# Kernel optimization log

Measured on AMD Instinct MI355X. Metric: run time of the kernel, lower is better.

## Reference

```python
import jax, jax.numpy as jnp
import numpy as np

LENGTH = 5
TOP_K = 5
POOL_SIZE = 60
EMBED_DIM = 768
MAP_SCALE = 0.1
MAX_NORM = 1.0 - 4e-3  # Poincare ball projection eps for float32 (geoopt convention)
EPS = 1e-12


def _l2_normalize(x):
    ss = jnp.sum(x * x, axis=-1, keepdims=True)
    return x * jax.lax.rsqrt(jnp.maximum(ss, EPS))


def _expmap0(u):
    # c = 1: expmap0(u) = tanh(||u||) * u / ||u||
    n = jnp.sqrt(jnp.maximum(jnp.sum(u * u, axis=-1, keepdims=True), 1e-15))
    return jnp.tanh(n) * u / n


def _proju0(x):
    # project onto the open unit ball
    n = jnp.sqrt(jnp.maximum(jnp.sum(x * x, axis=-1, keepdims=True), 1e-15))
    return jnp.where(n > MAX_NORM, x * (MAX_NORM / n), x)


def _map_to_ball(x):
    return _proju0(_expmap0(_l2_normalize(x) * MAP_SCALE))


def _mobius_add(x, y):
    # c = 1 Mobius addition, broadcasting over leading dims
    x2 = jnp.sum(x * x, axis=-1, keepdims=True)
    y2 = jnp.sum(y * y, axis=-1, keepdims=True)
    xy = jnp.sum(x * y, axis=-1, keepdims=True)
    num = (1.0 + 2.0 * xy + y2) * x + (1.0 - x2) * y
    den = 1.0 + 2.0 * xy + x2 * y2
    return num / jnp.maximum(den, 1e-15)


def _poincare_dist(x, y):
    # dist(x, y) = 2 * artanh(||(-x) mobius+ y||)  (c = 1)
    d = _mobius_add(-x, y)
    n = jnp.sqrt(jnp.maximum(jnp.sum(d * d, axis=-1), 1e-15))
    n = jnp.clip(n, 0.0, 1.0 - 1e-7)
    return 2.0 * jnp.arctanh(n)


def setup_inputs() -> dict:
    key = jax.random.key(0)
    k1, k2, k3 = jax.random.split(key, 3)
    x_embed = jax.random.normal(k1, (128, 512, EMBED_DIM), dtype=jnp.float32)
    prompt = jax.random.uniform(k2, (POOL_SIZE, LENGTH, EMBED_DIM), dtype=jnp.float32, minval=-1.0, maxval=1.0)
    prompt_key = jax.random.uniform(k3, (POOL_SIZE, EMBED_DIM), dtype=jnp.float32, minval=-1.0, maxval=1.0)
    return {"x_embed": x_embed, "prompt": prompt, "prompt_key": prompt_key}


def reference(x_embed, prompt, prompt_key):
    B = x_embed.shape[0]
    x_mean = jnp.mean(x_embed, axis=1)                      # [B, D]
    key_ball = _map_to_ball(prompt_key)                     # [P, D]
    q_ball = _map_to_ball(x_mean)                           # [B, D]
    dist = _poincare_dist(q_ball[:, None, :], key_ball[None, :, :])  # [B, P]
    similarity = -dist
    _, idx = jax.lax.top_k(similarity, TOP_K)               # [B, K]
    idx = jnp.sort(idx, axis=1)
    batched_prompt = prompt[idx].reshape(B, TOP_K * LENGTH, EMBED_DIM)
    selected_key = key_ball[idx]                            # [B, K, D]
    selected_dist = jnp.take_along_axis(dist, idx, axis=1)  # [B, K]
    reduce_sim = jnp.sum(selected_dist) / B
    prompted_embedding = jnp.concatenate([batched_prompt, x_embed], axis=1)
    return (prompted_embedding, reduce_sim, idx, similarity, selected_key)
```

## Files before the change

### kernel.cpp

```cpp
#include <hip/hip_runtime.h>

#define EMBED   768
#define EMBED4  192
#define POOL    60
#define BATCH   128
#define SEQ     512
#define TOPK    5
#define LEN     5
#define OUTROWS 537
#define NSLICE  16

#define SZ_PE   (128L*537L*768L)
#define OFF_RS  (SZ_PE)
#define OFF_IDX (OFF_RS + 1)
#define OFF_SIM (OFF_IDX + 640)
#define OFF_SK  (OFF_SIM + 7680)

#define WS_PARTIAL 0
#define WS_KEYBALL 1572864
#define WS_KEYY2   1618944

#define MAX_NORM_F 0.996f

__device__ __forceinline__ float block_reduce_256(float v, float* red) {
    int tid = threadIdx.x;
    #pragma unroll
    for (int m = 32; m >= 1; m >>= 1) v += __shfl_xor(v, m, 64);
    if ((tid & 63) == 0) red[tid >> 6] = v;
    __syncthreads();
    float total = red[0] + red[1] + red[2] + red[3];
    __syncthreads();
    return total;
}

__global__ __launch_bounds__(192) void mean_partial_copy(
        const float* __restrict__ x, float* __restrict__ out, float* __restrict__ partial) {
    const int slice = blockIdx.x, b = blockIdx.y, tid = threadIdx.x;
    const float4* __restrict__ x4 = (const float4*)x;
    float4* __restrict__ out4 = (float4*)out;
    float4* __restrict__ p4 = (float4*)partial;

    if (slice == 0 && b == 0 && tid == 0) out[OFF_RS] = 0.0f;

    float4 acc = make_float4(0.f, 0.f, 0.f, 0.f);
    const int rows = SEQ / NSLICE;
    const long ibase = ((long)b * SEQ + slice * rows) * EMBED4 + tid;
    const long obase = ((long)b * OUTROWS + 25 + slice * rows) * EMBED4 + tid;
    #pragma unroll 4
    for (int s = 0; s < rows; ++s) {
        float4 v = x4[ibase + (long)s * EMBED4];
        acc.x += v.x; acc.y += v.y; acc.z += v.z; acc.w += v.w;
        out4[obase + (long)s * EMBED4] = v;
    }
    p4[(long)(b * NSLICE + slice) * EMBED4 + tid] = acc;
}

__global__ __launch_bounds__(256) void keyball_kernel(
        const float* __restrict__ pkey, float* __restrict__ keyball, float* __restrict__ keyy2) {
    __shared__ float red[4];
    const int p = blockIdx.x, tid = threadIdx.x;
    float v[3];
    float ss = 0.f;
    #pragma unroll
    for (int j = 0; j < 3; ++j) { v[j] = pkey[p * EMBED + tid + 256 * j]; ss += v[j] * v[j]; }
    ss = block_reduce_256(ss, red);
    const float scale1 = rsqrtf(fmaxf(ss, 1e-12f)) * 0.1f;
    float su = 0.f;
    #pragma unroll
    for (int j = 0; j < 3; ++j) { v[j] *= scale1; su += v[j] * v[j]; }
    su = block_reduce_256(su, red);
    const float n = sqrtf(fmaxf(su, 1e-15f));
    const float f = tanhf(n) / n;
    float sb = 0.f;
    #pragma unroll
    for (int j = 0; j < 3; ++j) { v[j] *= f; sb += v[j] * v[j]; }
    sb = block_reduce_256(sb, red);
    const float n2 = sqrtf(fmaxf(sb, 1e-15f));
    const float g = (n2 > MAX_NORM_F) ? (MAX_NORM_F / n2) : 1.0f;
    #pragma unroll
    for (int j = 0; j < 3; ++j) keyball[p * EMBED + tid + 256 * j] = v[j] * g;
    if (tid == 0) keyy2[p] = sb * g * g;
}

__global__ __launch_bounds__(256) void topk_fused(
        const float* __restrict__ partial, const float* __restrict__ keyball,
        const float* __restrict__ keyy2, const float* __restrict__ prompt,
        float* __restrict__ out) {
    __shared__ float red[4];
    __shared__ float q[EMBED];
    __shared__ float xy[POOL];
    __shared__ float dist[POOL];
    __shared__ int sel_sh[TOPK];
    const int b = blockIdx.x, tid = threadIdx.x;

    float v[3];
    {
        const float inv = 1.0f / (float)SEQ;
        #pragma unroll
        for (int j = 0; j < 3; ++j) {
            const int col = tid + 256 * j;
            float s = 0.f;
            #pragma unroll
            for (int sl = 0; sl < NSLICE; ++sl)
                s += partial[(long)(b * NSLICE + sl) * EMBED + col];
            v[j] = s * inv;
        }
    }

    float ss = 0.f;
    #pragma unroll
    for (int j = 0; j < 3; ++j) ss += v[j] * v[j];
    ss = block_reduce_256(ss, red);
    const float scale1 = rsqrtf(fmaxf(ss, 1e-12f)) * 0.1f;
    float su = 0.f;
    #pragma unroll
    for (int j = 0; j < 3; ++j) { v[j] *= scale1; su += v[j] * v[j]; }
    su = block_reduce_256(su, red);
    const float n = sqrtf(fmaxf(su, 1e-15f));
    const float f = tanhf(n) / n;
    float sb = 0.f;
    #pragma unroll
    for (int j = 0; j < 3; ++j) { v[j] *= f; sb += v[j] * v[j]; }
    sb = block_reduce_256(sb, red);
    const float n2 = sqrtf(fmaxf(sb, 1e-15f));
    const float g = (n2 > MAX_NORM_F) ? (MAX_NORM_F / n2) : 1.0f;
    const float x2 = sb * g * g;
    #pragma unroll
    for (int j = 0; j < 3; ++j) q[tid + 256 * j] = v[j] * g;
    __syncthreads();

    const int wave = tid >> 6, lane = tid & 63;
    for (int p = wave; p < POOL; p += 4) {
        const float* __restrict__ kb = keyball + p * EMBED;
        float acc = 0.f;
        #pragma unroll
        for (int d = 0; d < EMBED; d += 64) acc += q[d + lane] * kb[d + lane];
        #pragma unroll
        for (int m = 32; m >= 1; m >>= 1) acc += __shfl_xor(acc, m, 64);
        if (lane == 0) xy[p] = acc;
    }
    __syncthreads();

    if (tid < POOL) {
        const float s = xy[tid];
        const float y2 = keyy2[tid];
        const float A = 1.0f - 2.0f * s + y2;
        const float B = 1.0f - x2;
        const float num2 = A * A * x2 + B * B * y2 - 2.0f * A * B * s;
        const float den = fmaxf(1.0f - 2.0f * s + x2 * y2, 1e-15f);
        float nn = sqrtf(fmaxf(num2 / (den * den), 1e-15f));
        nn = fminf(fmaxf(nn, 0.0f), 1.0f - 1e-7f);
        const float dd = logf((1.0f + nn) / (1.0f - nn));
        dist[tid] = dd;
        out[OFF_SIM + (long)b * POOL + tid] = -dd;
    }
    __syncthreads();

    if (tid == 0) {
        int sel[TOPK];
        unsigned long long mask = 0ULL;
        for (int k = 0; k < TOPK; ++k) {
            int best = 0; float bd = 1e30f;
            for (int p = 0; p < POOL; ++p) {
                if (mask & (1ULL << p)) continue;
                if (dist[p] < bd) { bd = dist[p]; best = p; }
            }
            mask |= 1ULL << best;
            sel[k] = best;
        }
        #pragma unroll
        for (int i = 0; i < TOPK; ++i)
            for (int j2 = i + 1; j2 < TOPK; ++j2)
                if (sel[j2] < sel[i]) { int t = sel[i]; sel[i] = sel[j2]; sel[j2] = t; }
        float sum = 0.f;
        for (int k = 0; k < TOPK; ++k) {
            sum += dist[sel[k]];
            out[OFF_IDX + (long)b * TOPK + k] = (float)sel[k];
            sel_sh[k] = sel[k];
        }
        atomicAdd(&out[OFF_RS], sum * (1.0f / 128.0f));
    }
    __syncthreads();

    for (int t = tid; t < TOPK * EMBED; t += 256) {
        const int k = t / EMBED, d = t - k * EMBED;
        out[OFF_SK + (long)b * TOPK * EMBED + t] = keyball[sel_sh[k] * EMBED + d];
    }

    {
        const float4* __restrict__ p4 = (const float4*)prompt;
        float4* __restrict__ o4 = (float4*)out;
        for (int t = tid; t < TOPK * LEN * EMBED4; t += 256) {
            const int r = t / EMBED4, c = t - r * EMBED4;
            const int k = r / LEN, l = r - k * LEN;
            const int pi = sel_sh[k];
            o4[((long)b * OUTROWS + r) * EMBED4 + c] = p4[((long)pi * LEN + l) * EMBED4 + c];
        }
    }
}

extern "C" void kernel_launch(void* const* d_in, const int* in_sizes, int n_in,
                              void* d_out, int out_size, void* d_ws, size_t ws_size,
                              hipStream_t stream) {
    const float* x      = (const float*)d_in[0];
    const float* prompt = (const float*)d_in[1];
    const float* pkey   = (const float*)d_in[2];
    float* out = (float*)d_out;
    float* ws  = (float*)d_ws;

    float* partial = ws + WS_PARTIAL;
    float* keyball = ws + WS_KEYBALL;
    float* keyy2   = ws + WS_KEYY2;

    hipLaunchKernelGGL(mean_partial_copy, dim3(NSLICE, 128), dim3(192), 0, stream, x, out, partial);
    hipLaunchKernelGGL(keyball_kernel,    dim3(60),          dim3(256), 0, stream, pkey, keyball, keyy2);
    hipLaunchKernelGGL(topk_fused,        dim3(128),         dim3(256), 0, stream,
                       partial, keyball, keyy2, prompt, out);
}
```

Baseline: 395.3 us.

## Use nontemporal batched loads/stores in copy and split gather into wide kernel

```diff
diff --git a/kernel.cpp b/kernel.cpp
--- a/kernel.cpp
+++ b/kernel.cpp
@@ -19,8 +19,11 @@
 #define WS_PARTIAL 0
 #define WS_KEYBALL 1572864
 #define WS_KEYY2   1618944
+#define WS_SEL     1619008
 
 #define MAX_NORM_F 0.996f
+
+typedef float fx4 __attribute__((ext_vector_type(4)));
 
 __device__ __forceinline__ float block_reduce_256(float v, float* red) {
     int tid = threadIdx.x;
@@ -36,21 +39,27 @@
 __global__ __launch_bounds__(192) void mean_partial_copy(
         const float* __restrict__ x, float* __restrict__ out, float* __restrict__ partial) {
     const int slice = blockIdx.x, b = blockIdx.y, tid = threadIdx.x;
-    const float4* __restrict__ x4 = (const float4*)x;
-    float4* __restrict__ out4 = (float4*)out;
-    float4* __restrict__ p4 = (float4*)partial;
+    const fx4* __restrict__ x4 = (const fx4*)x;
+    fx4* __restrict__ out4 = (fx4*)out;
+    fx4* __restrict__ p4 = (fx4*)partial;
 
     if (slice == 0 && b == 0 && tid == 0) out[OFF_RS] = 0.0f;
 
-    float4 acc = make_float4(0.f, 0.f, 0.f, 0.f);
+    fx4 acc = (fx4)(0.f);
     const int rows = SEQ / NSLICE;
     const long ibase = ((long)b * SEQ + slice * rows) * EMBED4 + tid;
     const long obase = ((long)b * OUTROWS + 25 + slice * rows) * EMBED4 + tid;
-    #pragma unroll 4
-    for (int s = 0; s < rows; ++s) {
-        float4 v = x4[ibase + (long)s * EMBED4];
-        acc.x += v.x; acc.y += v.y; acc.z += v.z; acc.w += v.w;
-        out4[obase + (long)s * EMBED4] = v;
+    #pragma unroll
+    for (int s0 = 0; s0 < rows; s0 += 8) {
+        fx4 v[8];
+        #pragma unroll
+        for (int i = 0; i < 8; ++i)
+            v[i] = __builtin_nontemporal_load(&x4[ibase + (long)(s0 + i) * EMBED4]);
+        #pragma unroll
+        for (int i = 0; i < 8; ++i) {
+            acc += v[i];
+            __builtin_nontemporal_store(v[i], &out4[obase + (long)(s0 + i) * EMBED4]);
+        }
     }
     p4[(long)(b * NSLICE + slice) * EMBED4 + tid] = acc;
 }
@@ -82,15 +91,13 @@
     if (tid == 0) keyy2[p] = sb * g * g;
 }
 
-__global__ __launch_bounds__(256) void topk_fused(
+__global__ __launch_bounds__(256) void topk_core(
         const float* __restrict__ partial, const float* __restrict__ keyball,
-        const float* __restrict__ keyy2, const float* __restrict__ prompt,
-        float* __restrict__ out) {
+        const float* __restrict__ keyy2, float* __restrict__ out, int* __restrict__ selw) {
     __shared__ float red[4];
     __shared__ float q[EMBED];
     __shared__ float xy[POOL];
     __shared__ float dist[POOL];
-    __shared__ int sel_sh[TOPK];
     const int b = blockIdx.x, tid = threadIdx.x;
 
     float v[3];
@@ -176,26 +183,29 @@
         for (int k = 0; k < TOPK; ++k) {
             sum += dist[sel[k]];
             out[OFF_IDX + (long)b * TOPK + k] = (float)sel[k];
-            sel_sh[k] = sel[k];
+            selw[b * TOPK + k] = sel[k];
         }
         atomicAdd(&out[OFF_RS], sum * (1.0f / 128.0f));
     }
-    __syncthreads();
-
-    for (int t = tid; t < TOPK * EMBED; t += 256) {
-        const int k = t / EMBED, d = t - k * EMBED;
-        out[OFF_SK + (long)b * TOPK * EMBED + t] = keyball[sel_sh[k] * EMBED + d];
-    }
-
-    {
-        const float4* __restrict__ p4 = (const float4*)prompt;
-        float4* __restrict__ o4 = (float4*)out;
-        for (int t = tid; t < TOPK * LEN * EMBED4; t += 256) {
-            const int r = t / EMBED4, c = t - r * EMBED4;
-            const int k = r / LEN, l = r - k * LEN;
-            const int pi = sel_sh[k];
-            o4[((long)b * OUTROWS + r) * EMBED4 + c] = p4[((long)pi * LEN + l) * EMBED4 + c];
-        }
+}
+
+__global__ __launch_bounds__(192) void gather_kernel(
+        const float* __restrict__ prompt, const float* __restrict__ keyball,
+        const int* __restrict__ selw, float* __restrict__ out) {
+    const int r = blockIdx.x, b = blockIdx.y, tid = threadIdx.x;
+    if (r < TOPK * LEN) {
+        const int k = r / LEN, l = r - k * LEN;
+        const int pi = selw[b * TOPK + k];
+        const float4* __restrict__ src = (const float4*)prompt + ((long)pi * LEN + l) * EMBED4;
+        float4* __restrict__ dst = (float4*)out + ((long)b * OUTROWS + r) * EMBED4;
+        dst[tid] = src[tid];
+    } else {
+        const int k = r - TOPK * LEN;
+        const int pi = selw[b * TOPK + k];
+        const float* __restrict__ src = keyball + (long)pi * EMBED;
+        float* __restrict__ dst = out + OFF_SK + ((long)b * TOPK + k) * EMBED;
+        #pragma unroll
+        for (int j = 0; j < 4; ++j) dst[tid + 192 * j] = src[tid + 192 * j];
     }
 }
 
@@ -211,9 +221,12 @@
     float* partial = ws + WS_PARTIAL;
     float* keyball = ws + WS_KEYBALL;
     float* keyy2   = ws + WS_KEYY2;
+    int*   selw    = (int*)(ws + WS_SEL);
 
     hipLaunchKernelGGL(mean_partial_copy, dim3(NSLICE, 128), dim3(192), 0, stream, x, out, partial);
     hipLaunchKernelGGL(keyball_kernel,    dim3(60),          dim3(256), 0, stream, pkey, keyball, keyy2);
-    hipLaunchKernelGGL(topk_fused,        dim3(128),         dim3(256), 0, stream,
-                       partial, keyball, keyy2, prompt, out);
-}
+    hipLaunchKernelGGL(topk_core,         dim3(128),         dim3(256), 0, stream,
+                       partial, keyball, keyy2, out, selw);
+    hipLaunchKernelGGL(gather_kernel,     dim3(30, 128),     dim3(192), 0, stream,
+                       prompt, keyball, selw, out);
+}
```

Result: faster. 377.6 us (-4.5%).
